# Kernel optimization log

Measured on AMD Instinct MI355X. Metric: run time of the kernel, lower is better.

## Reference

```python
import jax, jax.numpy as jnp
import numpy as np

D = 32
H = 64
B, N, M = 2, 512, 512


def setup_inputs() -> dict:
    key = jax.random.key(0)
    ks = jax.random.split(key, 6)
    s = 0.1  # modest init scale for MLP params
    return {
        "Q": jax.random.normal(ks[0], (B, N, D), dtype=jnp.float32),
        "K": jax.random.normal(ks[1], (B, M, D), dtype=jnp.float32),
        "w1": jax.random.normal(ks[2], (D, H), dtype=jnp.float32) * s,
        "b1": jax.random.normal(ks[3], (H,), dtype=jnp.float32) * s,
        "w2": jax.random.normal(ks[4], (H, D * D), dtype=jnp.float32) * s,
        "b2": jax.random.normal(ks[5], (D * D,), dtype=jnp.float32) * s,
    }


def _cholesky_factor(x, w1, b1, w2, b2):
    """L(x) with unit-ish softplus diagonal; x: [..., D] -> L: [..., D, D]."""
    h = jax.nn.silu(x @ w1 + b1)
    raw = h @ w2 + b2                      # [..., D*D]
    raw = 5.0 * jnp.tanh(raw / 5.0)        # soft clamp
    L = (raw + jnp.eye(D, dtype=x.dtype).reshape(-1)).reshape(x.shape[:-1] + (D, D))
    tril = jnp.tril(jnp.ones((D, D), dtype=x.dtype))
    diag = jnp.eye(D, dtype=x.dtype)
    L = L * tril
    L = L * (1.0 - diag) + (jax.nn.softplus(L) + 1e-4) * diag
    return L


def reference(Q, K, w1, b1, w2, b2):
    L_q = _cholesky_factor(Q, w1, b1, w2, b2)   # [B,N,D,D]
    L_k = _cholesky_factor(K, w1, b1, w2, b2)   # [B,M,D,D]
    delta = Q[:, :, None, :] - K[:, None, :, :]  # [B,N,M,D]
    # delta^T G_avg delta = 0.5 (||L_q^T delta||^2 + ||L_k^T delta||^2)
    vq = jnp.einsum('bnij,bnmi->bnmj', L_q, delta)  # L_q^T delta
    vk = jnp.einsum('bmij,bnmi->bnmj', L_k, delta)  # L_k^T delta
    dist_sq = 0.5 * (jnp.sum(vq * vq, axis=-1) + jnp.sum(vk * vk, axis=-1))
    return jnp.sqrt(jnp.clip(dist_sq, 1e-6, 1e6))
```

## Files before the change

### kernel.cpp

```cpp
#include <hip/hip_runtime.h>
#include <math.h>

namespace {
constexpr int KF  = 1152;
constexpr int RPB = 4;
}

typedef __bf16 v8bf __attribute__((ext_vector_type(8)));
typedef float  v4f  __attribute__((ext_vector_type(4)));

__device__ __forceinline__ unsigned short f2bf(float f) {
    union { float f; unsigned u; } v; v.f = f;
    unsigned r = v.u + 0x7FFFu + ((v.u >> 16) & 1u);
    return (unsigned short)(r >> 16);
}

__device__ __forceinline__ v8bf as_v8bf(uint4 u) {
    union { uint4 u; v8bf b; } c; c.u = u; return c.b;
}

__global__ __launch_bounds__(256) void k_feat(
    const float* __restrict__ Q, const float* __restrict__ K,
    const float* __restrict__ w1, const float* __restrict__ b1,
    const float* __restrict__ w2, const float* __restrict__ b2,
    unsigned short* __restrict__ featA, unsigned short* __restrict__ featB,
    float* __restrict__ cOut)
{
    __shared__ __attribute__((aligned(16))) float x_s[RPB][32];
    __shared__ __attribute__((aligned(16))) float h_s[RPB][64];
    __shared__ __attribute__((aligned(16))) float L_s[RPB][32][36];
    __shared__ __attribute__((aligned(16))) float G_s[RPB][528];
    __shared__ __attribute__((aligned(16))) float u_s[RPB][32];
    __shared__ unsigned short tri_s[528];

    const int t  = threadIdx.x;
    const int g0 = blockIdx.x * RPB;

    for (int pr = t; pr < 528; pr += 256) {
        int j = (int)((65.0f - sqrtf(4225.0f - 8.0f * (float)pr)) * 0.5f);
        while (j > 0 && j * (65 - j) / 2 > pr) --j;
        while ((j + 1) * (64 - j) / 2 <= pr) ++j;
        int i = j + (pr - j * (65 - j) / 2);
        tri_s[pr] = (unsigned short)((i << 8) | j);
    }
    if (t < RPB * 32) {
        int r = t >> 5, i = t & 31;
        int g = g0 + r;
        const float* src = (g < 1024) ? (Q + (size_t)g * 32)
                                      : (K + (size_t)(g - 1024) * 32);
        x_s[r][i] = src[i];
    }
    __syncthreads();

    {
        int r = t >> 6, j = t & 63;
        float z = b1[j];
        #pragma unroll
        for (int i = 0; i < 32; ++i) z = fmaf(x_s[r][i], w1[i * 64 + j], z);
        h_s[r][j] = z / (1.0f + __expf(-z));
    }
    __syncthreads();

    {
        const int p4 = t * 4;
        float acc[RPB][4];
        float4 bq = *(const float4*)&b2[p4];
        #pragma unroll
        for (int r = 0; r < RPB; ++r) {
            acc[r][0] = bq.x; acc[r][1] = bq.y; acc[r][2] = bq.z; acc[r][3] = bq.w;
        }
        for (int jb = 0; jb < 8; ++jb) {
            float h8[RPB][8];
            #pragma unroll
            for (int r = 0; r < RPB; ++r) {
                *(float4*)&h8[r][0] = *(const float4*)&h_s[r][jb * 8 + 0];
                *(float4*)&h8[r][4] = *(const float4*)&h_s[r][jb * 8 + 4];
            }
            #pragma unroll
            for (int jj = 0; jj < 8; ++jj) {
                float4 w = *(const float4*)&w2[(size_t)(jb * 8 + jj) * 1024 + p4];
                #pragma unroll
                for (int r = 0; r < RPB; ++r) {
                    acc[r][0] = fmaf(h8[r][jj], w.x, acc[r][0]);
                    acc[r][1] = fmaf(h8[r][jj], w.y, acc[r][1]);
                    acc[r][2] = fmaf(h8[r][jj], w.z, acc[r][2]);
                    acc[r][3] = fmaf(h8[r][jj], w.w, acc[r][3]);
                }
            }
        }
        const int i  = p4 >> 5;
        const int j0 = p4 & 31;
        #pragma unroll
        for (int r = 0; r < RPB; ++r) {
            float4 lv;
            float* lvp = (float*)&lv;
            #pragma unroll
            for (int e = 0; e < 4; ++e) {
                int j = j0 + e;
                float raw = acc[r][e];
                float ex = __expf(0.4f * raw);
                float c5 = 5.0f * (ex - 1.0f) / (ex + 1.0f);
                float val;
                if (i < j)       val = 0.0f;
                else if (i == j) { float z = c5 + 1.0f; val = log1pf(__expf(z)) + 1e-4f; }
                else             val = c5;
                lvp[e] = val;
            }
            *(float4*)&L_s[r][i][j0] = lv;
        }
    }
    __syncthreads();

    for (int idx = t; idx < RPB * 528; idx += 256) {
        int r  = idx / 528;
        int pr = idx - r * 528;
        int tv = tri_s[pr];
        int i = tv >> 8, j = tv & 255;
        const float* Li = &L_s[r][i][0];
        const float* Lj = &L_s[r][j][0];
        float s = 0.0f;
        int nf = (j + 1) >> 2;
        for (int q = 0; q < nf; ++q) {
            float4 a  = *(const float4*)&Li[q * 4];
            float4 bb = *(const float4*)&Lj[q * 4];
            s += a.x * bb.x + a.y * bb.y + a.z * bb.z + a.w * bb.w;
        }
        for (int tt = nf * 4; tt <= j; ++tt) s = fmaf(Li[tt], Lj[tt], s);
        G_s[r][pr] = s;
    }
    __syncthreads();

    if (t < RPB * 32) {
        int r = t >> 5, i = t & 31;
        float s = 0.0f;
        #pragma unroll
        for (int j = 0; j < 32; ++j) {
            float gv = (j <= i) ? G_s[r][j * (65 - j) / 2 + i - j]
                                : G_s[r][i * (65 - i) / 2 + j - i];
            s = fmaf(gv, x_s[r][j], s);
        }
        u_s[r][i] = s;
    }
    __syncthreads();

    if (t < RPB) {
        float s = 0.0f;
        #pragma unroll
        for (int i = 0; i < 32; ++i) s = fmaf(u_s[t][i], x_s[t][i], s);
        cOut[g0 + t] = s;
    }

    for (int idx = t; idx < RPB * (KF / 4); idx += 256) {
        int r   = idx / (KF / 4);
        int q   = idx - r * (KF / 4);
        int pos = q * 4;
        int g   = g0 + r;
        bool isA = (g < 1024);
        unsigned short* dst = isA ? (featA + (size_t)g * KF)
                                  : (featB + (size_t)(g - 1024) * KF);
        unsigned short ev[4];
        #pragma unroll
        for (int e = 0; e < 4; ++e) {
            int p = pos + e;
            float va;
            if (p < 1056) {
                int pr = (p < 528) ? p : p - 528;
                bool wantG = (p < 528) ? isA : !isA;
                int tv = tri_s[pr];
                int i = tv >> 8, j = tv & 255;
                float gv = G_s[r][pr] * ((i == j) ? 1.0f : 2.0f);
                float ov = x_s[r][i] * x_s[r][j];
                va = wantG ? gv : ov;
            } else if (p < 1088) {
                int i = p - 1056;
                va = isA ? u_s[r][i] : -2.0f * x_s[r][i];
            } else if (p < 1120) {
                int i = p - 1088;
                va = isA ? x_s[r][i] : -2.0f * u_s[r][i];
            } else {
                va = 0.0f;
            }
            ev[e] = f2bf(va);
        }
        uint2 w;
        w.x = (unsigned)ev[0] | ((unsigned)ev[1] << 16);
        w.y = (unsigned)ev[2] | ((unsigned)ev[3] << 16);
        *(uint2*)(dst + pos) = w;
    }
}

__global__ __launch_bounds__(256) void k_gemm(
    const unsigned short* __restrict__ featA,
    const unsigned short* __restrict__ featB,
    const float* __restrict__ cOut,
    float* __restrict__ out)
{
    __shared__ __attribute__((aligned(16))) float red[4][32][36];

    const int t    = threadIdx.x;
    const int lane = t & 63;
    const int w    = t >> 6;

    const int lin = blockIdx.x;
    const int swz = (lin & 7) * 64 + (lin >> 3);
    const int m0 = (swz & 15) * 32;
    const int n0 = ((swz >> 4) & 15) * 32;
    const int b  = swz >> 8;

    const int fr = lane & 15;
    const int fq = lane >> 4;
    const int kbase = w * 288 + fq * 8;

    const unsigned short* pA0 = featA + (size_t)(b * 512 + n0 + fr) * KF + kbase;
    const unsigned short* pA1 = pA0 + (size_t)16 * KF;
    const unsigned short* pB0 = featB + (size_t)(b * 512 + m0 + fr) * KF + kbase;
    const unsigned short* pB1 = pB0 + (size_t)16 * KF;

    v4f acc00 = {0,0,0,0}, acc01 = {0,0,0,0}, acc10 = {0,0,0,0}, acc11 = {0,0,0,0};

    uint4 bA0[4], bA1[4], bB0[4], bB1[4];
    #pragma unroll
    for (int s = 0; s < 4; ++s) {
        bA0[s] = *(const uint4*)(pA0 + s * 32);
        bA1[s] = *(const uint4*)(pA1 + s * 32);
        bB0[s] = *(const uint4*)(pB0 + s * 32);
        bB1[s] = *(const uint4*)(pB1 + s * 32);
    }

    #pragma unroll
    for (int s = 0; s < 9; ++s) {
        const int slot = s & 3;
        v8bf a0  = as_v8bf(bA0[slot]);
        v8bf a1  = as_v8bf(bA1[slot]);
        v8bf b0v = as_v8bf(bB0[slot]);
        v8bf b1v = as_v8bf(bB1[slot]);
        const int kn = s + 4;
        if (kn < 9) {
            bA0[slot] = *(const uint4*)(pA0 + kn * 32);
            bA1[slot] = *(const uint4*)(pA1 + kn * 32);
            bB0[slot] = *(const uint4*)(pB0 + kn * 32);
            bB1[slot] = *(const uint4*)(pB1 + kn * 32);
        }
        acc00 = __builtin_amdgcn_mfma_f32_16x16x32_bf16(a0, b0v, acc00, 0, 0, 0);
        acc01 = __builtin_amdgcn_mfma_f32_16x16x32_bf16(a0, b1v, acc01, 0, 0, 0);
        acc10 = __builtin_amdgcn_mfma_f32_16x16x32_bf16(a1, b0v, acc10, 0, 0, 0);
        acc11 = __builtin_amdgcn_mfma_f32_16x16x32_bf16(a1, b1v, acc11, 0, 0, 0);
    }

    #pragma unroll
    for (int v = 0; v < 4; ++v) {
        red[w][fq * 4 + v][fr]           = acc00[v];
        red[w][fq * 4 + v][fr + 16]      = acc01[v];
        red[w][16 + fq * 4 + v][fr]      = acc10[v];
        red[w][16 + fq * 4 + v][fr + 16] = acc11[v];
    }
    __syncthreads();

    const int n_l  = t >> 3;
    const int m_l0 = (t & 7) * 4;
    float4 s0 = *(const float4*)&red[0][n_l][m_l0];
    float4 s1 = *(const float4*)&red[1][n_l][m_l0];
    float4 s2 = *(const float4*)&red[2][n_l][m_l0];
    float4 s3 = *(const float4*)&red[3][n_l][m_l0];

    const int   n_g = n0 + n_l;
    const float cA  = cOut[b * 512 + n_g];
    const float4 cB = *(const float4*)&cOut[1024 + b * 512 + m0 + m_l0];

    float4 res;
    {
        float tot[4] = { s0.x + s1.x + s2.x + s3.x,
                         s0.y + s1.y + s2.y + s3.y,
                         s0.z + s1.z + s2.z + s3.z,
                         s0.w + s1.w + s2.w + s3.w };
        const float cb[4] = { cB.x, cB.y, cB.z, cB.w };
        float* rp = (float*)&res;
        #pragma unroll
        for (int e = 0; e < 4; ++e) {
            float dsq = 0.5f * (tot[e] + cA + cb[e]);
            dsq = fminf(fmaxf(dsq, 1e-6f), 1e6f);
            rp[e] = sqrtf(dsq);
        }
    }
    *(float4*)&out[((size_t)(b * 512 + n_g)) * 512 + m0 + m_l0] = res;
}

extern "C" void kernel_launch(void* const* d_in, const int* in_sizes, int n_in,
                              void* d_out, int out_size, void* d_ws, size_t ws_size,
                              hipStream_t stream)
{
    const float* Q  = (const float*)d_in[0];
    const float* K  = (const float*)d_in[1];
    const float* w1 = (const float*)d_in[2];
    const float* b1 = (const float*)d_in[3];
    const float* w2 = (const float*)d_in[4];
    const float* b2 = (const float*)d_in[5];
    float* out = (float*)d_out;

    unsigned short* featA = (unsigned short*)d_ws;
    unsigned short* featB = featA + (size_t)1024 * KF;
    float* cOut = (float*)(featB + (size_t)1024 * KF);

    k_feat<<<dim3(2048 / RPB), dim3(256), 0, stream>>>(Q, K, w1, b1, w2, b2, featA, featB, cOut);
    k_gemm<<<dim3(512), dim3(256), 0, stream>>>(featA, featB, cOut, out);
}
```

Baseline: 101.1 us.

## Fuse feature and GEMM kernels into one cooperative launch with grid sync

Merges the feature-building kernel and the bf16 MFMA distance GEMM into a single cooperative kernel. A grid-wide barrier separates the two phases, and both phases share one shared-memory union. This is meant to remove the second kernel launch and the gap between launches. In exchange it adds the cost of a grid sync and cooperative-launch overhead, and it requires all 512 blocks to be resident at once.

```diff
diff --git a/kernel.cpp b/kernel.cpp
--- a/kernel.cpp
+++ b/kernel.cpp
@@ -1,5 +1,8 @@
 #include <hip/hip_runtime.h>
+#include <hip/hip_cooperative_groups.h>
 #include <math.h>
+
+namespace cg = cooperative_groups;
 
 namespace {
 constexpr int KF  = 1152;
@@ -19,270 +22,289 @@
     union { uint4 u; v8bf b; } c; c.u = u; return c.b;
 }
 
-__global__ __launch_bounds__(256) void k_feat(
+
+struct P1 {
+    float x_s[RPB][32];
+    float h_s[RPB][64];
+    float L_s[RPB][32][36];
+    float G_s[RPB][528];
+    float u_s[RPB][32];
+    unsigned short tri_s[528];
+};
+struct P2 {
+    float red[4][32][36];
+};
+union Smem {
+    P1 p1;
+    P2 p2;
+};
+
+__global__ __launch_bounds__(256, 2) void k_fused(
     const float* __restrict__ Q, const float* __restrict__ K,
     const float* __restrict__ w1, const float* __restrict__ b1,
     const float* __restrict__ w2, const float* __restrict__ b2,
     unsigned short* __restrict__ featA, unsigned short* __restrict__ featB,
-    float* __restrict__ cOut)
+    float* __restrict__ cOut, float* __restrict__ out)
 {
-    __shared__ __attribute__((aligned(16))) float x_s[RPB][32];
-    __shared__ __attribute__((aligned(16))) float h_s[RPB][64];
-    __shared__ __attribute__((aligned(16))) float L_s[RPB][32][36];
-    __shared__ __attribute__((aligned(16))) float G_s[RPB][528];
-    __shared__ __attribute__((aligned(16))) float u_s[RPB][32];
-    __shared__ unsigned short tri_s[528];
-
-    const int t  = threadIdx.x;
-    const int g0 = blockIdx.x * RPB;
-
-    for (int pr = t; pr < 528; pr += 256) {
-        int j = (int)((65.0f - sqrtf(4225.0f - 8.0f * (float)pr)) * 0.5f);
-        while (j > 0 && j * (65 - j) / 2 > pr) --j;
-        while ((j + 1) * (64 - j) / 2 <= pr) ++j;
-        int i = j + (pr - j * (65 - j) / 2);
-        tri_s[pr] = (unsigned short)((i << 8) | j);
-    }
-    if (t < RPB * 32) {
-        int r = t >> 5, i = t & 31;
-        int g = g0 + r;
-        const float* src = (g < 1024) ? (Q + (size_t)g * 32)
-                                      : (K + (size_t)(g - 1024) * 32);
-        x_s[r][i] = src[i];
-    }
-    __syncthreads();
+    __shared__ __attribute__((aligned(16))) Smem smem;
+
+    const int t = threadIdx.x;
 
     {
-        int r = t >> 6, j = t & 63;
-        float z = b1[j];
-        #pragma unroll
-        for (int i = 0; i < 32; ++i) z = fmaf(x_s[r][i], w1[i * 64 + j], z);
-        h_s[r][j] = z / (1.0f + __expf(-z));
-    }
-    __syncthreads();
-
-    {
-        const int p4 = t * 4;
-        float acc[RPB][4];
-        float4 bq = *(const float4*)&b2[p4];
-        #pragma unroll
-        for (int r = 0; r < RPB; ++r) {
-            acc[r][0] = bq.x; acc[r][1] = bq.y; acc[r][2] = bq.z; acc[r][3] = bq.w;
-        }
-        for (int jb = 0; jb < 8; ++jb) {
-            float h8[RPB][8];
+        auto& x_s  = smem.p1.x_s;
+        auto& h_s  = smem.p1.h_s;
+        auto& L_s  = smem.p1.L_s;
+        auto& G_s  = smem.p1.G_s;
+        auto& u_s  = smem.p1.u_s;
+        auto& tri_s = smem.p1.tri_s;
+
+        const int g0 = blockIdx.x * RPB;
+
+        for (int pr = t; pr < 528; pr += 256) {
+            int j = (int)((65.0f - sqrtf(4225.0f - 8.0f * (float)pr)) * 0.5f);
+            while (j > 0 && j * (65 - j) / 2 > pr) --j;
+            while ((j + 1) * (64 - j) / 2 <= pr) ++j;
+            int i = j + (pr - j * (65 - j) / 2);
+            tri_s[pr] = (unsigned short)((i << 8) | j);
+        }
+        if (t < RPB * 32) {
+            int r = t >> 5, i = t & 31;
+            int g = g0 + r;
+            const float* src = (g < 1024) ? (Q + (size_t)g * 32)
+                                          : (K + (size_t)(g - 1024) * 32);
+            x_s[r][i] = src[i];
+        }
+        __syncthreads();
+
+        {
+            int r = t >> 6, j = t & 63;
+            float z = b1[j];
+            #pragma unroll
+            for (int i = 0; i < 32; ++i) z = fmaf(x_s[r][i], w1[i * 64 + j], z);
+            h_s[r][j] = z / (1.0f + __expf(-z));
+        }
+        __syncthreads();
+
+        {
+            const int p4 = t * 4;
+            float acc[RPB][4];
+            float4 bq = *(const float4*)&b2[p4];
             #pragma unroll
             for (int r = 0; r < RPB; ++r) {
-                *(float4*)&h8[r][0] = *(const float4*)&h_s[r][jb * 8 + 0];
-                *(float4*)&h8[r][4] = *(const float4*)&h_s[r][jb * 8 + 4];
-            }
-            #pragma unroll
-            for (int jj = 0; jj < 8; ++jj) {
-                float4 w = *(const float4*)&w2[(size_t)(jb * 8 + jj) * 1024 + p4];
+                acc[r][0] = bq.x; acc[r][1] = bq.y; acc[r][2] = bq.z; acc[r][3] = bq.w;
+            }
+            for (int jb = 0; jb < 8; ++jb) {
+                float h8[RPB][8];
                 #pragma unroll
                 for (int r = 0; r < RPB; ++r) {
-                    acc[r][0] = fmaf(h8[r][jj], w.x, acc[r][0]);
-                    acc[r][1] = fmaf(h8[r][jj], w.y, acc[r][1]);
-                    acc[r][2] = fmaf(h8[r][jj], w.z, acc[r][2]);
-                    acc[r][3] = fmaf(h8[r][jj], w.w, acc[r][3]);
+                    *(float4*)&h8[r][0] = *(const float4*)&h_s[r][jb * 8 + 0];
+                    *(float4*)&h8[r][4] = *(const float4*)&h_s[r][jb * 8 + 4];
                 }
-            }
-        }
-        const int i  = p4 >> 5;
-        const int j0 = p4 & 31;
+                #pragma unroll
+                for (int jj = 0; jj < 8; ++jj) {
+                    float4 w = *(const float4*)&w2[(size_t)(jb * 8 + jj) * 1024 + p4];
+                    #pragma unroll
+                    for (int r = 0; r < RPB; ++r) {
+                        acc[r][0] = fmaf(h8[r][jj], w.x, acc[r][0]);
+                        acc[r][1] = fmaf(h8[r][jj], w.y, acc[r][1]);
+                        acc[r][2] = fmaf(h8[r][jj], w.z, acc[r][2]);
+                        acc[r][3] = fmaf(h8[r][jj], w.w, acc[r][3]);
+                    }
+                }
+            }
+            const int i  = p4 >> 5;
+            const int j0 = p4 & 31;
+            #pragma unroll
+            for (int r = 0; r < RPB; ++r) {
+                float4 lv;
+                float* lvp = (float*)&lv;
+                #pragma unroll
+                for (int e = 0; e < 4; ++e) {
+                    int j = j0 + e;
+                    float raw = acc[r][e];
+                    float ex = __expf(0.4f * raw);
+                    float c5 = 5.0f * (ex - 1.0f) / (ex + 1.0f);
+                    float val;
+                    if (i < j)       val = 0.0f;
+                    else if (i == j) { float z = c5 + 1.0f; val = log1pf(__expf(z)) + 1e-4f; }
+                    else             val = c5;
+                    lvp[e] = val;
+                }
+                *(float4*)&L_s[r][i][j0] = lv;
+            }
+        }
+        __syncthreads();
+
+        for (int idx = t; idx < RPB * 528; idx += 256) {
+            int r  = idx / 528;
+            int pr = idx - r * 528;
+            int tv = tri_s[pr];
+            int i = tv >> 8, j = tv & 255;
+            const float* Li = &L_s[r][i][0];
+            const float* Lj = &L_s[r][j][0];
+            float s = 0.0f;
+            int nf = (j + 1) >> 2;
+            for (int q = 0; q < nf; ++q) {
+                float4 a  = *(const float4*)&Li[q * 4];
+                float4 bb = *(const float4*)&Lj[q * 4];
+                s += a.x * bb.x + a.y * bb.y + a.z * bb.z + a.w * bb.w;
+            }
+            for (int tt = nf * 4; tt <= j; ++tt) s = fmaf(Li[tt], Lj[tt], s);
+            G_s[r][pr] = s;
+        }
+        __syncthreads();
+
+        if (t < RPB * 32) {
+            int r = t >> 5, i = t & 31;
+            float s = 0.0f;
+            #pragma unroll
+            for (int j = 0; j < 32; ++j) {
+                float gv = (j <= i) ? G_s[r][j * (65 - j) / 2 + i - j]
+                                    : G_s[r][i * (65 - i) / 2 + j - i];
+                s = fmaf(gv, x_s[r][j], s);
+            }
+            u_s[r][i] = s;
+        }
+        __syncthreads();
+
+        if (t < RPB) {
+            float s = 0.0f;
+            #pragma unroll
+            for (int i = 0; i < 32; ++i) s = fmaf(u_s[t][i], x_s[t][i], s);
+            cOut[g0 + t] = s;
+        }
+
+        for (int idx = t; idx < RPB * (KF / 4); idx += 256) {
+            int r   = idx / (KF / 4);
+            int q   = idx - r * (KF / 4);
+            int pos = q * 4;
+            int g   = g0 + r;
+            bool isA = (g < 1024);
+            unsigned short* dst = isA ? (featA + (size_t)g * KF)
+                                      : (featB + (size_t)(g - 1024) * KF);
+            unsigned short ev[4];
+            #pragma unroll
+            for (int e = 0; e < 4; ++e) {
+                int p = pos + e;
+                float va;
+                if (p < 1056) {
+                    int pr = (p < 528) ? p : p - 528;
+                    bool wantG = (p < 528) ? isA : !isA;
+                    int tv = tri_s[pr];
+                    int i = tv >> 8, j = tv & 255;
+                    float gv = G_s[r][pr] * ((i == j) ? 1.0f : 2.0f);
+                    float ov = x_s[r][i] * x_s[r][j];
+                    va = wantG ? gv : ov;
+                } else if (p < 1088) {
+                    int i = p - 1056;
+                    va = isA ? u_s[r][i] : -2.0f * x_s[r][i];
+                } else if (p < 1120) {
+                    int i = p - 1088;
+                    va = isA ? x_s[r][i] : -2.0f * u_s[r][i];
+                } else {
+                    va = 0.0f;
+                }
+                ev[e] = f2bf(va);
+            }
+            uint2 w;
+            w.x = (unsigned)ev[0] | ((unsigned)ev[1] << 16);
+            w.y = (unsigned)ev[2] | ((unsigned)ev[3] << 16);
+            *(uint2*)(dst + pos) = w;
+        }
+    }
+
+    __threadfence();
+    cg::this_grid().sync();
+
+    {
+        auto& red = smem.p2.red;
+
+        const int lane = t & 63;
+        const int w    = t >> 6;
+
+        const int lin = blockIdx.x;
+        const int swz = (lin & 7) * 64 + (lin >> 3);
+        const int m0 = (swz & 15) * 32;
+        const int n0 = ((swz >> 4) & 15) * 32;
+        const int b  = swz >> 8;
+
+        const int fr = lane & 15;
+        const int fq = lane >> 4;
+        const int kbase = w * 288 + fq * 8;
+
+        const unsigned short* pA0 = featA + (size_t)(b * 512 + n0 + fr) * KF + kbase;
+        const unsigned short* pA1 = pA0 + (size_t)16 * KF;
+        const unsigned short* pB0 = featB + (size_t)(b * 512 + m0 + fr) * KF + kbase;
+        const unsigned short* pB1 = pB0 + (size_t)16 * KF;
+
+        v4f acc00 = {0,0,0,0}, acc01 = {0,0,0,0}, acc10 = {0,0,0,0}, acc11 = {0,0,0,0};
+
+        uint4 bA0[4], bA1[4], bB0[4], bB1[4];
         #pragma unroll
-        for (int r = 0; r < RPB; ++r) {
-            float4 lv;
-            float* lvp = (float*)&lv;
+        for (int s = 0; s < 4; ++s) {
+            bA0[s] = *(const uint4*)(pA0 + s * 32);
+            bA1[s] = *(const uint4*)(pA1 + s * 32);
+            bB0[s] = *(const uint4*)(pB0 + s * 32);
+            bB1[s] = *(const uint4*)(pB1 + s * 32);
+        }
+
+        #pragma unroll
+        for (int s = 0; s < 9; ++s) {
+            const int slot = s & 3;
+            v8bf a0  = as_v8bf(bA0[slot]);
+            v8bf a1  = as_v8bf(bA1[slot]);
+            v8bf b0v = as_v8bf(bB0[slot]);
+            v8bf b1v = as_v8bf(bB1[slot]);
+            const int kn = s + 4;
+            if (kn < 9) {
+                bA0[slot] = *(const uint4*)(pA0 + kn * 32);
+                bA1[slot] = *(const uint4*)(pA1 + kn * 32);
+                bB0[slot] = *(const uint4*)(pB0 + kn * 32);
+                bB1[slot] = *(const uint4*)(pB1 + kn * 32);
+            }
+            acc00 = __builtin_amdgcn_mfma_f32_16x16x32_bf16(a0, b0v, acc00, 0, 0, 0);
+            acc01 = __builtin_amdgcn_mfma_f32_16x16x32_bf16(a0, b1v, acc01, 0, 0, 0);
+            acc10 = __builtin_amdgcn_mfma_f32_16x16x32_bf16(a1, b0v, acc10, 0, 0, 0);
+            acc11 = __builtin_amdgcn_mfma_f32_16x16x32_bf16(a1, b1v, acc11, 0, 0, 0);
+        }
+
+        #pragma unroll
+        for (int v = 0; v < 4; ++v) {
+            red[w][fq * 4 + v][fr]           = acc00[v];
+            red[w][fq * 4 + v][fr + 16]      = acc01[v];
+            red[w][16 + fq * 4 + v][fr]      = acc10[v];
+            red[w][16 + fq * 4 + v][fr + 16] = acc11[v];
+        }
+        __syncthreads();
+
+        const int n_l  = t >> 3;
+        const int m_l0 = (t & 7) * 4;
+        float4 s0 = *(const float4*)&red[0][n_l][m_l0];
+        float4 s1 = *(const float4*)&red[1][n_l][m_l0];
+        float4 s2 = *(const float4*)&red[2][n_l][m_l0];
+        float4 s3 = *(const float4*)&red[3][n_l][m_l0];
+
+        const int   n_g = n0 + n_l;
+        const float cA  = cOut[b * 512 + n_g];
+        const float4 cB = *(const float4*)&cOut[1024 + b * 512 + m0 + m_l0];
+
+        float4 res;
+        {
+            float tot[4] = { s0.x + s1.x + s2.x + s3.x,
+                             s0.y + s1.y + s2.y + s3.y,
+                             s0.z + s1.z + s2.z + s3.z,
+                             s0.w + s1.w + s2.w + s3.w };
+            const float cb[4] = { cB.x, cB.y, cB.z, cB.w };
+            float* rp = (float*)&res;
             #pragma unroll
             for (int e = 0; e < 4; ++e) {
-                int j = j0 + e;
-                float raw = acc[r][e];
-                float ex = __expf(0.4f * raw);
-                float c5 = 5.0f * (ex - 1.0f) / (ex + 1.0f);
-                float val;
-                if (i < j)       val = 0.0f;
-                else if (i == j) { float z = c5 + 1.0f; val = log1pf(__expf(z)) + 1e-4f; }
-                else             val = c5;
-                lvp[e] = val;
-            }
-            *(float4*)&L_s[r][i][j0] = lv;
-        }
+                float dsq = 0.5f * (tot[e] + cA + cb[e]);
+                dsq = fminf(fmaxf(dsq, 1e-6f), 1e6f);
+                rp[e] = sqrtf(dsq);
+            }
+        }
+        *(float4*)&out[((size_t)(b * 512 + n_g)) * 512 + m0 + m_l0] = res;
     }
-    __syncthreads();
-
-    for (int idx = t; idx < RPB * 528; idx += 256) {
-        int r  = idx / 528;
-        int pr = idx - r * 528;
-        int tv = tri_s[pr];
-        int i = tv >> 8, j = tv & 255;
-        const float* Li = &L_s[r][i][0];
-        const float* Lj = &L_s[r][j][0];
-        float s = 0.0f;
-        int nf = (j + 1) >> 2;
-        for (int q = 0; q < nf; ++q) {
-            float4 a  = *(const float4*)&Li[q * 4];
-            float4 bb = *(const float4*)&Lj[q * 4];
-            s += a.x * bb.x + a.y * bb.y + a.z * bb.z + a.w * bb.w;
-        }
-        for (int tt = nf * 4; tt <= j; ++tt) s = fmaf(Li[tt], Lj[tt], s);
-        G_s[r][pr] = s;
-    }
-    __syncthreads();
-
-    if (t < RPB * 32) {
-        int r = t >> 5, i = t & 31;
-        float s = 0.0f;
-        #pragma unroll
-        for (int j = 0; j < 32; ++j) {
-            float gv = (j <= i) ? G_s[r][j * (65 - j) / 2 + i - j]
-                                : G_s[r][i * (65 - i) / 2 + j - i];
-            s = fmaf(gv, x_s[r][j], s);
-        }
-        u_s[r][i] = s;
-    }
-    __syncthreads();
-
-    if (t < RPB) {
-        float s = 0.0f;
-        #pragma unroll
-        for (int i = 0; i < 32; ++i) s = fmaf(u_s[t][i], x_s[t][i], s);
-        cOut[g0 + t] = s;
-    }
-
-    for (int idx = t; idx < RPB * (KF / 4); idx += 256) {
-        int r   = idx / (KF / 4);
-        int q   = idx - r * (KF / 4);
-        int pos = q * 4;
-        int g   = g0 + r;
-        bool isA = (g < 1024);
-        unsigned short* dst = isA ? (featA + (size_t)g * KF)
-                                  : (featB + (size_t)(g - 1024) * KF);
-        unsigned short ev[4];
-        #pragma unroll
-        for (int e = 0; e < 4; ++e) {
-            int p = pos + e;
-            float va;
-            if (p < 1056) {
-                int pr = (p < 528) ? p : p - 528;
-                bool wantG = (p < 528) ? isA : !isA;
-                int tv = tri_s[pr];
-                int i = tv >> 8, j = tv & 255;
-                float gv = G_s[r][pr] * ((i == j) ? 1.0f : 2.0f);
-                float ov = x_s[r][i] * x_s[r][j];
-                va = wantG ? gv : ov;
-            } else if (p < 1088) {
-                int i = p - 1056;
-                va = isA ? u_s[r][i] : -2.0f * x_s[r][i];
-            } else if (p < 1120) {
-                int i = p - 1088;
-                va = isA ? x_s[r][i] : -2.0f * u_s[r][i];
-            } else {
-                va = 0.0f;
-            }
-            ev[e] = f2bf(va);
-        }
-        uint2 w;
-        w.x = (unsigned)ev[0] | ((unsigned)ev[1] << 16);
-        w.y = (unsigned)ev[2] | ((unsigned)ev[3] << 16);
-        *(uint2*)(dst + pos) = w;
-    }
-}
-
-__global__ __launch_bounds__(256) void k_gemm(
-    const unsigned short* __restrict__ featA,
-    const unsigned short* __restrict__ featB,
-    const float* __restrict__ cOut,
-    float* __restrict__ out)
-{
-    __shared__ __attribute__((aligned(16))) float red[4][32][36];
-
-    const int t    = threadIdx.x;
-    const int lane = t & 63;
-    const int w    = t >> 6;
-
-    const int lin = blockIdx.x;
-    const int swz = (lin & 7) * 64 + (lin >> 3);
-    const int m0 = (swz & 15) * 32;
-    const int n0 = ((swz >> 4) & 15) * 32;
-    const int b  = swz >> 8;
-
-    const int fr = lane & 15;
-    const int fq = lane >> 4;
-    const int kbase = w * 288 + fq * 8;
-
-    const unsigned short* pA0 = featA + (size_t)(b * 512 + n0 + fr) * KF + kbase;
-    const unsigned short* pA1 = pA0 + (size_t)16 * KF;
-    const unsigned short* pB0 = featB + (size_t)(b * 512 + m0 + fr) * KF + kbase;
-    const unsigned short* pB1 = pB0 + (size_t)16 * KF;
-
-    v4f acc00 = {0,0,0,0}, acc01 = {0,0,0,0}, acc10 = {0,0,0,0}, acc11 = {0,0,0,0};
-
-    uint4 bA0[4], bA1[4], bB0[4], bB1[4];
-    #pragma unroll
-    for (int s = 0; s < 4; ++s) {
-        bA0[s] = *(const uint4*)(pA0 + s * 32);
-        bA1[s] = *(const uint4*)(pA1 + s * 32);
-        bB0[s] = *(const uint4*)(pB0 + s * 32);
-        bB1[s] = *(const uint4*)(pB1 + s * 32);
-    }
-
-    #pragma unroll
-    for (int s = 0; s < 9; ++s) {
-        const int slot = s & 3;
-        v8bf a0  = as_v8bf(bA0[slot]);
-        v8bf a1  = as_v8bf(bA1[slot]);
-        v8bf b0v = as_v8bf(bB0[slot]);
-        v8bf b1v = as_v8bf(bB1[slot]);
-        const int kn = s + 4;
-        if (kn < 9) {
-            bA0[slot] = *(const uint4*)(pA0 + kn * 32);
-            bA1[slot] = *(const uint4*)(pA1 + kn * 32);
-            bB0[slot] = *(const uint4*)(pB0 + kn * 32);
-            bB1[slot] = *(const uint4*)(pB1 + kn * 32);
-        }
-        acc00 = __builtin_amdgcn_mfma_f32_16x16x32_bf16(a0, b0v, acc00, 0, 0, 0);
-        acc01 = __builtin_amdgcn_mfma_f32_16x16x32_bf16(a0, b1v, acc01, 0, 0, 0);
-        acc10 = __builtin_amdgcn_mfma_f32_16x16x32_bf16(a1, b0v, acc10, 0, 0, 0);
-        acc11 = __builtin_amdgcn_mfma_f32_16x16x32_bf16(a1, b1v, acc11, 0, 0, 0);
-    }
-
-    #pragma unroll
-    for (int v = 0; v < 4; ++v) {
-        red[w][fq * 4 + v][fr]           = acc00[v];
-        red[w][fq * 4 + v][fr + 16]      = acc01[v];
-        red[w][16 + fq * 4 + v][fr]      = acc10[v];
-        red[w][16 + fq * 4 + v][fr + 16] = acc11[v];
-    }
-    __syncthreads();
-
-    const int n_l  = t >> 3;
-    const int m_l0 = (t & 7) * 4;
-    float4 s0 = *(const float4*)&red[0][n_l][m_l0];
-    float4 s1 = *(const float4*)&red[1][n_l][m_l0];
-    float4 s2 = *(const float4*)&red[2][n_l][m_l0];
-    float4 s3 = *(const float4*)&red[3][n_l][m_l0];
-
-    const int   n_g = n0 + n_l;
-    const float cA  = cOut[b * 512 + n_g];
-    const float4 cB = *(const float4*)&cOut[1024 + b * 512 + m0 + m_l0];
-
-    float4 res;
-    {
-        float tot[4] = { s0.x + s1.x + s2.x + s3.x,
-                         s0.y + s1.y + s2.y + s3.y,
-                         s0.z + s1.z + s2.z + s3.z,
-                         s0.w + s1.w + s2.w + s3.w };
-        const float cb[4] = { cB.x, cB.y, cB.z, cB.w };
-        float* rp = (float*)&res;
-        #pragma unroll
-        for (int e = 0; e < 4; ++e) {
-            float dsq = 0.5f * (tot[e] + cA + cb[e]);
-            dsq = fminf(fmaxf(dsq, 1e-6f), 1e6f);
-            rp[e] = sqrtf(dsq);
-        }
-    }
-    *(float4*)&out[((size_t)(b * 512 + n_g)) * 512 + m0 + m_l0] = res;
 }
 
 extern "C" void kernel_launch(void* const* d_in, const int* in_sizes, int n_in,
@@ -301,6 +323,8 @@
     unsigned short* featB = featA + (size_t)1024 * KF;
     float* cOut = (float*)(featB + (size_t)1024 * KF);
 
-    k_feat<<<dim3(2048 / RPB), dim3(256), 0, stream>>>(Q, K, w1, b1, w2, b2, featA, featB, cOut);
-    k_gemm<<<dim3(512), dim3(256), 0, stream>>>(featA, featB, cOut, out);
-}
+    void* args[] = { (void*)&Q, (void*)&K, (void*)&w1, (void*)&b1,
+                     (void*)&w2, (void*)&b2, (void*)&featA, (void*)&featB,
+                     (void*)&cOut, (void*)&out };
+    hipLaunchCooperativeKernel(k_fused, dim3(512), dim3(256), args, 0, stream);
+}
```

Result: slower. 179.0 us (+77.0%).

## Double-buffer w2 chunks into LDS via async global-to-LDS loads

Applied to the files above, without the earlier changes.

The second MLP layer in the feature kernel now streams w2 in 4-row chunks into a double-buffered shared-memory tile using global_load_lds, prefetching the next chunk while the current one is consumed. The aim is to hide global-memory latency on the w2 reads and replace direct global loads with LDS reads. In exchange it adds 32KB of LDS per block, which can lower occupancy, and a barrier per chunk. Correctness relies on the async LDS writes being waited on before the barrier.

```diff
diff --git a/kernel.cpp b/kernel.cpp
--- a/kernel.cpp
+++ b/kernel.cpp
@@ -17,6 +17,13 @@
 
 __device__ __forceinline__ v8bf as_v8bf(uint4 u) {
     union { uint4 u; v8bf b; } c; c.u = u; return c.b;
+}
+
+__device__ __forceinline__ void g2l16(const float* g, float* l) {
+    __builtin_amdgcn_global_load_lds(
+        (const __attribute__((address_space(1))) void*)g,
+        (__attribute__((address_space(3))) void*)l,
+        16, 0, 0);
 }
 
 __global__ __launch_bounds__(256) void k_feat(
@@ -31,10 +38,21 @@
     __shared__ __attribute__((aligned(16))) float L_s[RPB][32][36];
     __shared__ __attribute__((aligned(16))) float G_s[RPB][528];
     __shared__ __attribute__((aligned(16))) float u_s[RPB][32];
+    __shared__ __attribute__((aligned(16))) float wbuf[2][4 * 1024];
     __shared__ unsigned short tri_s[528];
 
-    const int t  = threadIdx.x;
-    const int g0 = blockIdx.x * RPB;
+    const int t    = threadIdx.x;
+    const int lane = t & 63;
+    const int wv   = t >> 6;
+    const int g0   = blockIdx.x * RPB;
+
+    {
+        #pragma unroll
+        for (int k = 0; k < 4; ++k) {
+            int q = wv * 4 + k;
+            g2l16(w2 + (size_t)q * 256 + lane * 4, &wbuf[0][q * 256]);
+        }
+    }
 
     for (int pr = t; pr < 528; pr += 256) {
         int j = (int)((65.0f - sqrtf(4225.0f - 8.0f * (float)pr)) * 0.5f);
@@ -69,24 +87,35 @@
         for (int r = 0; r < RPB; ++r) {
             acc[r][0] = bq.x; acc[r][1] = bq.y; acc[r][2] = bq.z; acc[r][3] = bq.w;
         }
-        for (int jb = 0; jb < 8; ++jb) {
-            float h8[RPB][8];
+        for (int c = 0; c < 16; ++c) {
+            const int buf = c & 1;
+            if (c < 15) {
+                #pragma unroll
+                for (int k = 0; k < 4; ++k) {
+                    int q = wv * 4 + k;
+                    g2l16(w2 + (size_t)(c + 1) * 4096 + q * 256 + lane * 4,
+                          &wbuf[buf ^ 1][q * 256]);
+                }
+            }
+            float4 h4[RPB];
             #pragma unroll
-            for (int r = 0; r < RPB; ++r) {
-                *(float4*)&h8[r][0] = *(const float4*)&h_s[r][jb * 8 + 0];
-                *(float4*)&h8[r][4] = *(const float4*)&h_s[r][jb * 8 + 4];
-            }
+            for (int r = 0; r < RPB; ++r)
+                h4[r] = *(const float4*)&h_s[r][c * 4];
+            const float* hp[RPB];
             #pragma unroll
-            for (int jj = 0; jj < 8; ++jj) {
-                float4 w = *(const float4*)&w2[(size_t)(jb * 8 + jj) * 1024 + p4];
+            for (int jr = 0; jr < 4; ++jr) {
+                float4 wq = *(const float4*)&wbuf[buf][jr * 1024 + p4];
                 #pragma unroll
                 for (int r = 0; r < RPB; ++r) {
-                    acc[r][0] = fmaf(h8[r][jj], w.x, acc[r][0]);
-                    acc[r][1] = fmaf(h8[r][jj], w.y, acc[r][1]);
-                    acc[r][2] = fmaf(h8[r][jj], w.z, acc[r][2]);
-                    acc[r][3] = fmaf(h8[r][jj], w.w, acc[r][3]);
+                    float hv = ((const float*)&h4[r])[jr];
+                    acc[r][0] = fmaf(hv, wq.x, acc[r][0]);
+                    acc[r][1] = fmaf(hv, wq.y, acc[r][1]);
+                    acc[r][2] = fmaf(hv, wq.z, acc[r][2]);
+                    acc[r][3] = fmaf(hv, wq.w, acc[r][3]);
                 }
             }
+            (void)hp;
+            if (c < 15) __syncthreads();
         }
         const int i  = p4 >> 5;
         const int j0 = p4 & 31;
```

Result: slower. 106.3 us (+5.2%).

## Split MLP feature kernel into a dedicated tiled raw-output kernel

Applied to the files above, without the earlier changes.

Moves the two-layer MLP out of the per-row feature kernel into a separate kernel that handles 32 rows per block across four column tiles, so each w2 load is reused by 8 rows per thread instead of 4. The raw MLP outputs are written to workspace and read back by the remaining feature kernel, which now does only the Cholesky/feature build. This cuts repeated w2 traffic across 512 blocks, at the cost of an extra launch and an 8 MB round trip of raw values through global memory.

```diff
diff --git a/kernel.cpp b/kernel.cpp
--- a/kernel.cpp
+++ b/kernel.cpp
@@ -19,15 +19,95 @@
     union { uint4 u; v8bf b; } c; c.u = u; return c.b;
 }
 
-__global__ __launch_bounds__(256) void k_feat(
+__global__ __launch_bounds__(256) void k_raw(
     const float* __restrict__ Q, const float* __restrict__ K,
     const float* __restrict__ w1, const float* __restrict__ b1,
     const float* __restrict__ w2, const float* __restrict__ b2,
+    float* __restrict__ rawOut)
+{
+    __shared__ __attribute__((aligned(16))) float x_s[32][32];
+    __shared__ __attribute__((aligned(16))) float h_s[32][64];
+
+    const int t    = threadIdx.x;
+    const int lane = t & 63;
+    const int wv   = t >> 6;
+    const int gr0  = blockIdx.x * 32;
+    const int c0   = blockIdx.y * 256;
+
+    {
+        int r  = t >> 3;
+        int i4 = (t & 7) * 4;
+        int g  = gr0 + r;
+        const float* src = (g < 1024) ? (Q + (size_t)g * 32)
+                                      : (K + (size_t)(g - 1024) * 32);
+        *(float4*)&x_s[r][i4] = *(const float4*)&src[i4];
+    }
+    __syncthreads();
+
+    {
+        const int j  = lane;
+        const int r0 = wv * 8;
+        float bj = b1[j];
+        float z[8];
+        #pragma unroll
+        for (int r = 0; r < 8; ++r) z[r] = bj;
+        for (int i = 0; i < 32; ++i) {
+            float wij = w1[i * 64 + j];
+            #pragma unroll
+            for (int r = 0; r < 8; ++r) z[r] = fmaf(x_s[r0 + r][i], wij, z[r]);
+        }
+        #pragma unroll
+        for (int r = 0; r < 8; ++r)
+            h_s[r0 + r][j] = z[r] / (1.0f + __expf(-z[r]));
+    }
+    __syncthreads();
+
+    {
+        const int p  = c0 + lane * 4;
+        const int r0 = wv * 8;
+        float4 bq = *(const float4*)&b2[p];
+        float acc[8][4];
+        #pragma unroll
+        for (int r = 0; r < 8; ++r) {
+            acc[r][0] = bq.x; acc[r][1] = bq.y; acc[r][2] = bq.z; acc[r][3] = bq.w;
+        }
+        for (int kq = 0; kq < 16; ++kq) {
+            float4 wrow[4];
+            #pragma unroll
+            for (int kk = 0; kk < 4; ++kk)
+                wrow[kk] = *(const float4*)&w2[(size_t)(kq * 4 + kk) * 1024 + p];
+            float4 hq[8];
+            #pragma unroll
+            for (int r = 0; r < 8; ++r)
+                hq[r] = *(const float4*)&h_s[r0 + r][kq * 4];
+            #pragma unroll
+            for (int kk = 0; kk < 4; ++kk) {
+                #pragma unroll
+                for (int r = 0; r < 8; ++r) {
+                    float hv = ((const float*)&hq[r])[kk];
+                    acc[r][0] = fmaf(hv, wrow[kk].x, acc[r][0]);
+                    acc[r][1] = fmaf(hv, wrow[kk].y, acc[r][1]);
+                    acc[r][2] = fmaf(hv, wrow[kk].z, acc[r][2]);
+                    acc[r][3] = fmaf(hv, wrow[kk].w, acc[r][3]);
+                }
+            }
+        }
+        #pragma unroll
+        for (int r = 0; r < 8; ++r) {
+            float4 o;
+            o.x = acc[r][0]; o.y = acc[r][1]; o.z = acc[r][2]; o.w = acc[r][3];
+            *(float4*)&rawOut[(size_t)(gr0 + r0 + r) * 1024 + p] = o;
+        }
+    }
+}
+
+__global__ __launch_bounds__(256) void k_rest(
+    const float* __restrict__ Q, const float* __restrict__ K,
+    const float* __restrict__ rawIn,
     unsigned short* __restrict__ featA, unsigned short* __restrict__ featB,
     float* __restrict__ cOut)
 {
     __shared__ __attribute__((aligned(16))) float x_s[RPB][32];
-    __shared__ __attribute__((aligned(16))) float h_s[RPB][64];
     __shared__ __attribute__((aligned(16))) float L_s[RPB][32][36];
     __shared__ __attribute__((aligned(16))) float G_s[RPB][528];
     __shared__ __attribute__((aligned(16))) float u_s[RPB][32];
@@ -50,54 +130,21 @@
                                       : (K + (size_t)(g - 1024) * 32);
         x_s[r][i] = src[i];
     }
-    __syncthreads();
-
-    {
-        int r = t >> 6, j = t & 63;
-        float z = b1[j];
-        #pragma unroll
-        for (int i = 0; i < 32; ++i) z = fmaf(x_s[r][i], w1[i * 64 + j], z);
-        h_s[r][j] = z / (1.0f + __expf(-z));
-    }
-    __syncthreads();
 
     {
         const int p4 = t * 4;
-        float acc[RPB][4];
-        float4 bq = *(const float4*)&b2[p4];
-        #pragma unroll
-        for (int r = 0; r < RPB; ++r) {
-            acc[r][0] = bq.x; acc[r][1] = bq.y; acc[r][2] = bq.z; acc[r][3] = bq.w;
-        }
-        for (int jb = 0; jb < 8; ++jb) {
-            float h8[RPB][8];
-            #pragma unroll
-            for (int r = 0; r < RPB; ++r) {
-                *(float4*)&h8[r][0] = *(const float4*)&h_s[r][jb * 8 + 0];
-                *(float4*)&h8[r][4] = *(const float4*)&h_s[r][jb * 8 + 4];
-            }
-            #pragma unroll
-            for (int jj = 0; jj < 8; ++jj) {
-                float4 w = *(const float4*)&w2[(size_t)(jb * 8 + jj) * 1024 + p4];
-                #pragma unroll
-                for (int r = 0; r < RPB; ++r) {
-                    acc[r][0] = fmaf(h8[r][jj], w.x, acc[r][0]);
-                    acc[r][1] = fmaf(h8[r][jj], w.y, acc[r][1]);
-                    acc[r][2] = fmaf(h8[r][jj], w.z, acc[r][2]);
-                    acc[r][3] = fmaf(h8[r][jj], w.w, acc[r][3]);
-                }
-            }
-        }
         const int i  = p4 >> 5;
         const int j0 = p4 & 31;
         #pragma unroll
         for (int r = 0; r < RPB; ++r) {
+            float4 rq = *(const float4*)&rawIn[(size_t)(g0 + r) * 1024 + p4];
+            const float* ra = (const float*)&rq;
             float4 lv;
             float* lvp = (float*)&lv;
             #pragma unroll
             for (int e = 0; e < 4; ++e) {
                 int j = j0 + e;
-                float raw = acc[r][e];
+                float raw = ra[e];
                 float ex = __expf(0.4f * raw);
                 float c5 = 5.0f * (ex - 1.0f) / (ex + 1.0f);
                 float val;
@@ -300,7 +347,9 @@
     unsigned short* featA = (unsigned short*)d_ws;
     unsigned short* featB = featA + (size_t)1024 * KF;
     float* cOut = (float*)(featB + (size_t)1024 * KF);
-
-    k_feat<<<dim3(2048 / RPB), dim3(256), 0, stream>>>(Q, K, w1, b1, w2, b2, featA, featB, cOut);
+    float* raw  = cOut + 2048;
+
+    k_raw<<<dim3(64, 4), dim3(256), 0, stream>>>(Q, K, w1, b1, w2, b2, raw);
+    k_rest<<<dim3(2048 / RPB), dim3(256), 0, stream>>>(Q, K, raw, featA, featB, cOut);
     k_gemm<<<dim3(512), dim3(256), 0, stream>>>(featA, featB, cOut, out);
 }
```

Result: slower. 114.0 us (+12.7%).
